# Kernel tuning notes

Measured on AMD Instinct MI355X. Metric: run time of the kernel, lower is better.

Reference implementation:

```python
import jax, jax.numpy as jnp
import numpy as np

EPS = 1e-8  # torch nn.CosineSimilarity default eps

def setup_inputs() -> dict:
    key = jax.random.key(0)
    kx, ky = jax.random.split(key)
    x = jax.random.normal(kx, (8, 2048, 512), dtype=jnp.float32)
    y = jax.random.normal(ky, (8, 2048, 512), dtype=jnp.float32)
    return {"x": x, "y": y}

def reference(x, y):
    # cosine(x_i, y_j) = <x_i, y_j> / max(||x_i|| * ||y_j||, eps)
    # GEMM form instead of the O(n^2 d) broadcast-expand.
    dots = jnp.einsum('bnd,bmd->bnm', x, y)            # [bs, n, n]
    xn = jnp.linalg.norm(x, axis=-1)                   # [bs, n]
    yn = jnp.linalg.norm(y, axis=-1)                   # [bs, n]
    denom = jnp.maximum(xn[:, :, None] * yn[:, None, :], EPS)
    return dots / denom
```

## Files before the change

### kernel.cpp

```cpp
#include <hip/hip_runtime.h>

#define BATCH 8
#define NROW  2048
#define DIM   512
#define BM 128
#define BN 128
#define BK 32

typedef __bf16 bf16x8 __attribute__((ext_vector_type(8)));
typedef float  f32x4  __attribute__((ext_vector_type(4)));

typedef __attribute__((address_space(3))) void       lds_t;
typedef const __attribute__((address_space(1))) void gmem_t;

__device__ __forceinline__ unsigned short f2bf(float f) {
    unsigned int u = __float_as_uint(f);
    u += 0x7FFFu + ((u >> 16) & 1u);
    return (unsigned short)(u >> 16);
}

__global__ __launch_bounds__(256) void prep_kernel(
    const float* __restrict__ x, const float* __restrict__ y,
    unsigned short* __restrict__ xbf, unsigned short* __restrict__ ybf,
    float* __restrict__ rxn, float* __restrict__ ryn)
{
    const int wave = threadIdx.x >> 6;
    const int lane = threadIdx.x & 63;
    const int row  = blockIdx.x * 4 + wave;

    const float* src; unsigned short* dst; float* rn;
    if (blockIdx.y == 0) { src = x; dst = xbf; rn = rxn; }
    else                 { src = y; dst = ybf; rn = ryn; }

    const float4* s4 = (const float4*)(src + (size_t)row * DIM);
    ushort4*      d4 = (ushort4*)(dst + (size_t)row * DIM);

    float ss = 0.f;
#pragma unroll
    for (int h = 0; h < 2; ++h) {
        float4 v = s4[h * 64 + lane];
        ss += v.x * v.x + v.y * v.y + v.z * v.z + v.w * v.w;
        ushort4 o;
        o.x = f2bf(v.x); o.y = f2bf(v.y); o.z = f2bf(v.z); o.w = f2bf(v.w);
        d4[h * 64 + lane] = o;
    }
#pragma unroll
    for (int off = 32; off; off >>= 1) ss += __shfl_xor(ss, off, 64);
    if (lane == 0) rn[row] = 1.0f / sqrtf(ss);
}

__global__ __launch_bounds__(256) void gemm_kernel(
    const __bf16* __restrict__ xbf, const __bf16* __restrict__ ybf,
    const float* __restrict__ rxn, const float* __restrict__ ryn,
    float* __restrict__ out)
{
    __shared__ __bf16 As[BM * BK];
    __shared__ __bf16 Bs[BN * BK];

    const int b    = blockIdx.y;
    const int bm   = blockIdx.x & 15;
    const int bn   = blockIdx.x >> 4;
    const int tid  = threadIdx.x;
    const int wave = tid >> 6;
    const int lane = tid & 63;
    const int wr   = wave >> 1;
    const int wc   = wave & 1;

    const __bf16* Ab = xbf + ((size_t)b * NROW + bm * BM) * DIM;
    const __bf16* Bb = ybf + ((size_t)b * NROW + bn * BN) * DIM;

    const int sr  = wave * 32 + (lane >> 2);
    const int sc  = (lane & 3) * 8;

    f32x4 acc[4][4] = {};

    for (int k0 = 0; k0 < DIM; k0 += BK) {
        __builtin_amdgcn_global_load_lds(
            (gmem_t*)(Ab + (size_t)sr * DIM + k0 + sc),
            (lds_t*)(As + (wave * 32) * BK), 16, 0, 0);
        __builtin_amdgcn_global_load_lds(
            (gmem_t*)(Ab + (size_t)(sr + 16) * DIM + k0 + sc),
            (lds_t*)(As + (wave * 32 + 16) * BK), 16, 0, 0);
        __builtin_amdgcn_global_load_lds(
            (gmem_t*)(Bb + (size_t)sr * DIM + k0 + sc),
            (lds_t*)(Bs + (wave * 32) * BK), 16, 0, 0);
        __builtin_amdgcn_global_load_lds(
            (gmem_t*)(Bb + (size_t)(sr + 16) * DIM + k0 + sc),
            (lds_t*)(Bs + (wave * 32 + 16) * BK), 16, 0, 0);

        __syncthreads();

        bf16x8 af[4], bfr[4];
#pragma unroll
        for (int m = 0; m < 4; ++m)
            af[m] = *(const bf16x8*)(As + (wr * 64 + m * 16 + (lane & 15)) * BK + (lane >> 4) * 8);
#pragma unroll
        for (int n = 0; n < 4; ++n)
            bfr[n] = *(const bf16x8*)(Bs + (wc * 64 + n * 16 + (lane & 15)) * BK + (lane >> 4) * 8);

#pragma unroll
        for (int m = 0; m < 4; ++m)
#pragma unroll
            for (int n = 0; n < 4; ++n)
                acc[m][n] = __builtin_amdgcn_mfma_f32_16x16x32_bf16(
                    af[m], bfr[n], acc[m][n], 0, 0, 0);

        __syncthreads();
    }

    const int col = lane & 15;
    const int r4  = (lane >> 4) * 4;
    const int gmb = bm * BM + wr * 64;
    const int gnb = bn * BN + wc * 64;
    float* C = out + (size_t)b * NROW * NROW;
    const float* rxb = rxn + b * NROW;
    const float* ryb = ryn + b * NROW;

#pragma unroll
    for (int n = 0; n < 4; ++n) {
        const float ry = ryb[gnb + n * 16 + col];
#pragma unroll
        for (int m = 0; m < 4; ++m) {
#pragma unroll
            for (int j = 0; j < 4; ++j) {
                const int gm = gmb + m * 16 + r4 + j;
                C[(size_t)gm * NROW + gnb + n * 16 + col] =
                    acc[m][n][j] * rxb[gm] * ry;
            }
        }
    }
}

extern "C" void kernel_launch(void* const* d_in, const int* in_sizes, int n_in,
                              void* d_out, int out_size, void* d_ws, size_t ws_size,
                              hipStream_t stream)
{
    const float* x = (const float*)d_in[0];
    const float* y = (const float*)d_in[1];
    float* out = (float*)d_out;

    char* ws = (char*)d_ws;
    unsigned short* xbf = (unsigned short*)ws;
    unsigned short* ybf = (unsigned short*)(ws + ((size_t)16 << 20));
    float* rxn = (float*)(ws + ((size_t)32 << 20));
    float* ryn = rxn + BATCH * NROW;

    prep_kernel<<<dim3(4096, 2), 256, 0, stream>>>(x, y, xbf, ybf, rxn, ryn);
    gemm_kernel<<<dim3(256, BATCH), 256, 0, stream>>>(
        (const __bf16*)xbf, (const __bf16*)ybf, rxn, ryn, out);
}
```

Measured before the change: 228.5 us.

## Rewrite GEMM as 256x256 tile, 8-wave, double-buffered pipelined MFMA kernel

Replaces the 128x128 single-buffered GEMM with a 256x256 tile per 512-thread workgroup and a 128 KB dynamic LDS double buffer. Global-to-LDS loads are issued phase by phase, interleaved with MFMA blocks, and controlled by explicit vmcnt waits, barriers and setprio. The LDS layout is XOR-swizzled to avoid bank conflicts, and the block index is remapped to change how tiles are assigned across the grid. The intent is to hide memory latency, cut LDS traffic per MFMA and improve operand reuse, at the cost of more registers, lower occupancy and fragile hand scheduling.

```diff
diff --git a/kernel.cpp b/kernel.cpp
--- a/kernel.cpp
+++ b/kernel.cpp
@@ -3,9 +3,6 @@
 #define BATCH 8
 #define NROW  2048
 #define DIM   512
-#define BM 128
-#define BN 128
-#define BK 32
 
 typedef __bf16 bf16x8 __attribute__((ext_vector_type(8)));
 typedef float  f32x4  __attribute__((ext_vector_type(4)));
@@ -49,84 +46,117 @@
     if (lane == 0) rn[row] = 1.0f / sqrtf(ss);
 }
 
-__global__ __launch_bounds__(256) void gemm_kernel(
+
+#define STAGE(Xp, Xi, K, T)                                                  \
+  { char* hb_ = sm + (((((T) & 1) << 2) | ((Xi) << 1) | (K)) << 14);         \
+    __builtin_amdgcn_global_load_lds(                                        \
+      (gmem_t*)((Xp) + (size_t)vr0 * DIM + (T) * 64 + (K) * 32 + vc),        \
+      (lds_t*)(hb_ + wave * 1024), 16, 0, 0);                                \
+    __builtin_amdgcn_global_load_lds(                                        \
+      (gmem_t*)((Xp) + (size_t)vr1 * DIM + (T) * 64 + (K) * 32 + vc),        \
+      (lds_t*)(hb_ + 8192 + wave * 1024), 16, 0, 0); }
+
+#define LDSA(M, KS, PAR) \
+  (*(const bf16x8*)(sm + ((((PAR) << 2) | (KS)) << 14) + ((wm * 8 + (M)) << 10) + rb))
+#define LDSB(N, KS, PAR) \
+  (*(const bf16x8*)(sm + ((((PAR) << 2) | 2 | (KS)) << 14) + ((wn * 4 + (N)) << 10) + rb))
+
+#define PHASE(PAR, MH, KS, READB, STAGE_STMT, VM_STMT)                       \
+  { __builtin_amdgcn_sched_barrier(0);                                       \
+    bf16x8 a0 = LDSA((MH)*4+0, KS, PAR), a1 = LDSA((MH)*4+1, KS, PAR),       \
+           a2 = LDSA((MH)*4+2, KS, PAR), a3 = LDSA((MH)*4+3, KS, PAR);       \
+    if (READB) { bfr[0] = LDSB(0, KS, PAR); bfr[1] = LDSB(1, KS, PAR);       \
+                 bfr[2] = LDSB(2, KS, PAR); bfr[3] = LDSB(3, KS, PAR); }     \
+    STAGE_STMT;                                                              \
+    __builtin_amdgcn_s_barrier();                                            \
+    asm volatile("s_waitcnt lgkmcnt(0)" ::: "memory");                       \
+    VM_STMT;                                                                 \
+    __builtin_amdgcn_sched_barrier(0);                                       \
+    __builtin_amdgcn_s_setprio(1);                                           \
+    _Pragma("unroll")                                                        \
+    for (int n = 0; n < 4; ++n) {                                            \
+      acc[(MH)*4+0][n] = __builtin_amdgcn_mfma_f32_16x16x32_bf16(a0, bfr[n], acc[(MH)*4+0][n], 0, 0, 0); \
+      acc[(MH)*4+1][n] = __builtin_amdgcn_mfma_f32_16x16x32_bf16(a1, bfr[n], acc[(MH)*4+1][n], 0, 0, 0); \
+      acc[(MH)*4+2][n] = __builtin_amdgcn_mfma_f32_16x16x32_bf16(a2, bfr[n], acc[(MH)*4+2][n], 0, 0, 0); \
+      acc[(MH)*4+3][n] = __builtin_amdgcn_mfma_f32_16x16x32_bf16(a3, bfr[n], acc[(MH)*4+3][n], 0, 0, 0); \
+    }                                                                        \
+    __builtin_amdgcn_s_setprio(0);                                           \
+    __builtin_amdgcn_sched_barrier(0);                                       \
+    __builtin_amdgcn_s_barrier(); }
+
+#define VM6 asm volatile("s_waitcnt vmcnt(6)" ::: "memory")
+#define VM0 asm volatile("s_waitcnt vmcnt(0)" ::: "memory")
+
+__global__ __launch_bounds__(512) void gemm_kernel(
     const __bf16* __restrict__ xbf, const __bf16* __restrict__ ybf,
     const float* __restrict__ rxn, const float* __restrict__ ryn,
     float* __restrict__ out)
 {
-    __shared__ __bf16 As[BM * BK];
-    __shared__ __bf16 Bs[BN * BK];
+    extern __shared__ char sm[];
+    const int tid  = threadIdx.x;
+    const int lane = tid & 63;
+    const int wave = tid >> 6;
+    const int wm   = wave >> 2;
+    const int wn   = wave & 3;
 
-    const int b    = blockIdx.y;
-    const int bm   = blockIdx.x & 15;
-    const int bn   = blockIdx.x >> 4;
-    const int tid  = threadIdx.x;
-    const int wave = tid >> 6;
-    const int lane = tid & 63;
-    const int wr   = wave >> 1;
-    const int wc   = wave & 1;
+    const int bid = blockIdx.x;
+    const int wg  = (bid & 7) * 64 + (bid >> 3);
+    const int b   = wg >> 6;
+    const int bm  = (wg >> 3) & 7;
+    const int bn  = wg & 7;
 
-    const __bf16* Ab = xbf + ((size_t)b * NROW + bm * BM) * DIM;
-    const __bf16* Bb = ybf + ((size_t)b * NROW + bn * BN) * DIM;
+    const __bf16* Ap = xbf + ((size_t)b * NROW + bm * 256) * DIM;
+    const __bf16* Bp = ybf + ((size_t)b * NROW + bn * 256) * DIM;
 
-    const int sr  = wave * 32 + (lane >> 2);
-    const int sc  = (lane & 3) * 8;
+    const int vr0 = wave * 16 + (lane >> 2);
+    const int vr1 = vr0 + 128;
+    const int vc  = ((lane & 3) * 8) ^ ((lane & 32) ? 16 : 0);
+    const int rb  = (lane & 15) * 64 + (((lane >> 4) * 16) ^ ((lane & 8) ? 32 : 0));
 
-    f32x4 acc[4][4] = {};
+    STAGE(Bp, 1, 0, 0) STAGE(Ap, 0, 0, 0) STAGE(Bp, 1, 1, 0) STAGE(Ap, 0, 1, 0)
+    STAGE(Bp, 1, 0, 1) STAGE(Ap, 0, 0, 1) STAGE(Bp, 1, 1, 1)
+    VM6;
+    __builtin_amdgcn_sched_barrier(0);
+    __builtin_amdgcn_s_barrier();
 
-    for (int k0 = 0; k0 < DIM; k0 += BK) {
-        __builtin_amdgcn_global_load_lds(
-            (gmem_t*)(Ab + (size_t)sr * DIM + k0 + sc),
-            (lds_t*)(As + (wave * 32) * BK), 16, 0, 0);
-        __builtin_amdgcn_global_load_lds(
-            (gmem_t*)(Ab + (size_t)(sr + 16) * DIM + k0 + sc),
-            (lds_t*)(As + (wave * 32 + 16) * BK), 16, 0, 0);
-        __builtin_amdgcn_global_load_lds(
-            (gmem_t*)(Bb + (size_t)sr * DIM + k0 + sc),
-            (lds_t*)(Bs + (wave * 32) * BK), 16, 0, 0);
-        __builtin_amdgcn_global_load_lds(
-            (gmem_t*)(Bb + (size_t)(sr + 16) * DIM + k0 + sc),
-            (lds_t*)(Bs + (wave * 32 + 16) * BK), 16, 0, 0);
+    f32x4 acc[8][4] = {};
+    bf16x8 bfr[4];
 
-        __syncthreads();
-
-        bf16x8 af[4], bfr[4];
-#pragma unroll
-        for (int m = 0; m < 4; ++m)
-            af[m] = *(const bf16x8*)(As + (wr * 64 + m * 16 + (lane & 15)) * BK + (lane >> 4) * 8);
-#pragma unroll
-        for (int n = 0; n < 4; ++n)
-            bfr[n] = *(const bf16x8*)(Bs + (wc * 64 + n * 16 + (lane & 15)) * BK + (lane >> 4) * 8);
-
-#pragma unroll
-        for (int m = 0; m < 4; ++m)
-#pragma unroll
-            for (int n = 0; n < 4; ++n)
-                acc[m][n] = __builtin_amdgcn_mfma_f32_16x16x32_bf16(
-                    af[m], bfr[n], acc[m][n], 0, 0, 0);
-
-        __syncthreads();
+    for (int i = 0; i < 4; ++i) {
+        const int t1 = 2 * i + 1, t2 = 2 * i + 2, t3 = 2 * i + 3;
+        const bool full = (i < 3);
+        PHASE(0, 0, 0, 1, STAGE(Ap, 0, 1, t1), )
+        PHASE(0, 1, 0, 0, if (full) STAGE(Bp, 1, 0, t2), )
+        PHASE(0, 0, 1, 1, if (full) STAGE(Ap, 0, 0, t2), )
+        PHASE(0, 1, 1, 0, if (full) STAGE(Bp, 1, 1, t2), if (full) { VM6; } else { VM0; })
+        PHASE(1, 0, 0, 1, if (full) STAGE(Ap, 0, 1, t2), )
+        PHASE(1, 1, 0, 0, if (full) STAGE(Bp, 1, 0, t3), )
+        PHASE(1, 0, 1, 1, if (full) STAGE(Ap, 0, 0, t3), )
+        PHASE(1, 1, 1, 0, if (full) STAGE(Bp, 1, 1, t3), if (full) { VM6; })
     }
 
     const int col = lane & 15;
     const int r4  = (lane >> 4) * 4;
-    const int gmb = bm * BM + wr * 64;
-    const int gnb = bn * BN + wc * 64;
+    const int gm0 = bm * 256 + wm * 128;
+    const int gn0 = bn * 256 + wn * 64;
     float* C = out + (size_t)b * NROW * NROW;
     const float* rxb = rxn + b * NROW;
     const float* ryb = ryn + b * NROW;
 
+    float ryv[4];
 #pragma unroll
-    for (int n = 0; n < 4; ++n) {
-        const float ry = ryb[gnb + n * 16 + col];
+    for (int n = 0; n < 4; ++n) ryv[n] = ryb[gn0 + n * 16 + col];
+
 #pragma unroll
-        for (int m = 0; m < 4; ++m) {
+    for (int m = 0; m < 8; ++m) {
 #pragma unroll
-            for (int j = 0; j < 4; ++j) {
-                const int gm = gmb + m * 16 + r4 + j;
-                C[(size_t)gm * NROW + gnb + n * 16 + col] =
-                    acc[m][n][j] * rxb[gm] * ry;
-            }
+        for (int j = 0; j < 4; ++j) {
+            const int gm = gm0 + m * 16 + r4 + j;
+            const float rx = rxb[gm];
+            float* Crow = C + (size_t)gm * NROW + gn0;
+#pragma unroll
+            for (int n = 0; n < 4; ++n)
+                Crow[n * 16 + col] = acc[m][n][j] * rx * ryv[n];
         }
     }
 }
@@ -145,7 +175,14 @@
     float* rxn = (float*)(ws + ((size_t)32 << 20));
     float* ryn = rxn + BATCH * NROW;
 
+    static bool attr_done = false;
+    if (!attr_done) {
+        hipFuncSetAttribute((const void*)gemm_kernel,
+                            hipFuncAttributeMaxDynamicSharedMemorySize, 131072);
+        attr_done = true;
+    }
+
     prep_kernel<<<dim3(4096, 2), 256, 0, stream>>>(x, y, xbf, ybf, rxn, ryn);
-    gemm_kernel<<<dim3(256, BATCH), 256, 0, stream>>>(
+    gemm_kernel<<<dim3(512), 512, 131072, stream>>>(
         (const __bf16*)xbf, (const __bf16*)ybf, rxn, ryn, out);
 }
```

Result: faster. 215.6 us (median of 2 runs) (-5.7%).
